# Kernel optimization log

Measured on AMD Instinct MI355X. Metric: run time of the kernel, lower is better.

Reference implementation:

```python
import jax, jax.numpy as jnp
import numpy as np
from jax.scipy.linalg import expm

B_SZ, T, INPUT_D = 32, 1024, 256
MEMORY_D, ORDER, THETA, HIDDEN = 8, 256, 1024.0, 512


def _lmu_matrices(order, theta):
    # Continuous-time Legendre system, then zero-order-hold discretization
    Q = np.arange(order, dtype=np.float64)
    R = (2 * Q + 1)[:, None] / theta
    j, i = np.meshgrid(Q, Q)
    Ac = np.where(i < j, -1.0, (-1.0) ** (i - j + 1)) * R
    Bc = (-1.0) ** Q[:, None] * R
    # ZOH via matrix exponential of the augmented system [[A,B],[0,0]]
    M = np.zeros((order + 1, order + 1))
    M[:order, :order] = Ac
    M[:order, order:] = Bc
    Md = np.asarray(expm(jnp.asarray(M)))
    Ad, Bd = Md[:order, :order], Md[:order, order:]
    # Stored transposed, as in LMUCell.build (used as right-multiplies)
    return Ad.T.astype(np.float32), Bd.T.astype(np.float32)  # (order,order), (1,order)


def setup_inputs() -> dict:
    key = jax.random.key(0)
    k1, k2, k3 = jax.random.split(key, 3)
    A, B = _lmu_matrices(ORDER, THETA)
    hidden_in = MEMORY_D * ORDER
    # glorot-uniform-like scales
    s_k = np.sqrt(6.0 / (INPUT_D + MEMORY_D)).astype(np.float32)
    s_h = np.sqrt(6.0 / (hidden_in + HIDDEN)).astype(np.float32)
    return {
        "x": jax.random.normal(k1, (B_SZ, T, INPUT_D), dtype=jnp.float32),
        "kernel": jax.random.uniform(k2, (INPUT_D, MEMORY_D), jnp.float32, -s_k, s_k),
        "Wh": jax.random.uniform(k3, (hidden_in, HIDDEN), jnp.float32, -s_h, s_h),
        "bh": jnp.zeros((HIDDEN,), jnp.float32),
        "A": jnp.asarray(A),
        "B": jnp.asarray(B),
    }


def reference(x, kernel, Wh, bh, A, B):
    # Encode all timesteps at once: u_t = x_t @ kernel  -> (B, T, memory_d)
    U = jnp.einsum("bti,im->btm", x, kernel)
    m0 = jnp.zeros((x.shape[0], MEMORY_D, ORDER), x.dtype)
    Brow = B[0]  # (order,)

    def step(m, u):
        # m: (B, memory_d, order); per LMUCell: m = m @ A + u[...,None] @ B
        m = jnp.einsum("bdo,op->bdp", m, A) + u[:, :, None] * Brow
        return m, m

    _, ms = jax.lax.scan(step, m0, jnp.swapaxes(U, 0, 1))  # (T, B, md, order)
    ms = jnp.swapaxes(ms, 0, 1).reshape(x.shape[0], x.shape[1], MEMORY_D * ORDER)
    # hidden cell: Dense(tanh) applied to memory at every step (return_sequences)
    return jnp.tanh(ms @ Wh + bh)  # (B, T, HIDDEN)
```

## Files before the change

### kernel.cpp

```cpp
#include <hip/hip_runtime.h>
#include <cstdint>
#include <cstddef>

constexpr int BSZ = 32;
constexpr int T   = 1024;
constexpr int ID  = 256;
constexpr int MD  = 8;
constexpr int ORD = 256;
constexpr int HID = 512;
constexpr int BD  = BSZ * MD;
constexpr int CH  = 64;
constexpr int NQ  = T / CH;
constexpr int DO  = MD * ORD;
constexpr int OO  = ORD * ORD;
constexpr int KTOT24 = CH + ORD;

typedef unsigned short ushort_t;
typedef __attribute__((ext_vector_type(8))) short bf16x8;
typedef __attribute__((ext_vector_type(8))) unsigned short us8;
typedef __attribute__((ext_vector_type(4))) float f32x4;

__device__ inline ushort_t f2bf(float f) {
    union { float f; uint32_t u; } v; v.f = f;
    uint32_t r = v.u + 0x7fffu + ((v.u >> 16) & 1u);
    return (ushort_t)(r >> 16);
}

__device__ inline void gl_lds16(const void* g, void* l) {
    __builtin_amdgcn_global_load_lds(
        (const __attribute__((address_space(1))) void*)g,
        (__attribute__((address_space(3))) void*)l, 16, 0, 0);
}

constexpr size_t AL = 256;
constexpr size_t alup(size_t x) { return (x + AL - 1) & ~(AL - 1); }
constexpr size_t OFF_U2   = 0;
constexpr size_t OFF_P    = alup(OFF_U2   + (size_t)BD * T * 4);
constexpr size_t OFF_APOW = alup(OFF_P    + (size_t)CH * ORD * 4);
constexpr size_t OFF_MQ   = alup(OFF_APOW + (size_t)(CH + 1) * OO * 4);
constexpr size_t OFF_LEND = alup(OFF_MQ   + (size_t)NQ * BD * ORD * 4);
constexpr size_t OFF_U2B  = alup(OFF_LEND + (size_t)NQ * BD * ORD * 4);
constexpr size_t OFF_PTRB = alup(OFF_U2B  + (size_t)BD * T * 2);
constexpr size_t OFF_APB  = alup(OFF_PTRB + (size_t)CH * ORD * CH * 2);
constexpr size_t OFF_WHBT = alup(OFF_APB  + (size_t)CH * ORD * ORD * 2);
constexpr size_t OFF_MQB  = alup(OFF_WHBT + (size_t)HID * DO * 2);
constexpr size_t OFF_MBUF = alup(OFF_MQB  + (size_t)NQ * BD * ORD * 2);

__global__ __launch_bounds__(256) void k_prep0(const float* __restrict__ x,
                                               const float* __restrict__ kern,
                                               float* __restrict__ U2,
                                               ushort_t* __restrict__ U2b,
                                               const float* __restrict__ A,
                                               float* __restrict__ Apow,
                                               ushort_t* __restrict__ Apb,
                                               const float* __restrict__ Wh,
                                               ushort_t* __restrict__ Whbt,
                                               const float* __restrict__ Brow,
                                               float* __restrict__ P) {
    __shared__ __align__(16) char sm[32 * (ID + 1) * 4 + ID * MD * 4];
    const int bid = blockIdx.x;
    const int tid = threadIdx.x;

    if (bid < 1024) {
        float (*xs)[ID + 1] = (float (*)[ID + 1])sm;
        float (*ks)[MD]     = (float (*)[MD])(sm + 32 * (ID + 1) * 4);
        const int b  = bid / (T / 32);
        const int t0 = (bid % (T / 32)) * 32;
        for (int i = tid; i < ID * MD; i += 256) ks[i / MD][i % MD] = kern[i];
        const float* xp = x + ((size_t)b * T + t0) * ID;
        for (int i = tid; i < (32 * ID) / 4; i += 256) {
            float4 v = ((const float4*)xp)[i];
            int r = i >> 6, c = (i & 63) * 4;
            xs[r][c] = v.x; xs[r][c + 1] = v.y; xs[r][c + 2] = v.z; xs[r][c + 3] = v.w;
        }
        __syncthreads();
        const int d  = tid / 32;
        const int tl = tid % 32;
        float acc = 0.f;
        #pragma unroll 8
        for (int i = 0; i < ID; ++i) acc += xs[tl][i] * ks[i][d];
        size_t idx = ((size_t)b * MD + d) * T + t0 + tl;
        U2[idx]  = acc;
        U2b[idx] = f2bf(acc);
    } else if (bid < 1088) {
        float (*t)[33] = (float (*)[33])sm;
        const int i2 = bid - 1024;
        const int o0 = (i2 & 7) * 32, p0 = (i2 >> 3) * 32;
        const int tx = tid & 31, ty = tid >> 5;
        #pragma unroll
        for (int p = 0; p < 4; ++p) {
            int r = ty + p * 8;
            float v = A[(size_t)(p0 + r) * ORD + o0 + tx];
            Apow[OO + (size_t)(p0 + r) * ORD + o0 + tx] = v;
            t[r][tx] = v;
        }
        __syncthreads();
        #pragma unroll
        for (int p = 0; p < 4; ++p) {
            int r = ty + p * 8;
            Apb[(size_t)(o0 + r) * ORD + p0 + tx] = f2bf(t[tx][r]);
        }
    } else if (bid < 2112) {
        float (*t)[33] = (float (*)[33])sm;
        const int i2 = bid - 1088;
        const int k0 = (i2 & 63) * 32, h0 = (i2 >> 6) * 32;
        const int tx = tid & 31, ty = tid >> 5;
        #pragma unroll
        for (int p = 0; p < 4; ++p) {
            int r = ty + p * 8;
            t[r][tx] = Wh[(size_t)(k0 + r) * HID + h0 + tx];
        }
        __syncthreads();
        #pragma unroll
        for (int p = 0; p < 4; ++p) {
            int r = ty + p * 8;
            Whbt[(size_t)(h0 + r) * DO + k0 + tx] = f2bf(t[tx][r]);
        }
    } else {
        P[tid] = Brow[tid];
    }
}


__device__ void pow_body(char* sm, int bid, int tid,
                         float* Apow, ushort_t* Apb, int n) {
    float (*As)[132] = (float (*)[132])sm;
    float (*Bs)[68]  = (float (*)[68])(sm + 33792);
    ushort_t (*tr)[72] = (ushort_t (*)[72])(sm + 68608);
    const int z    = bid >> 4;
    const int row0 = ((bid >> 2) & 3) * 64;
    const int col0 = (bid & 3) * 64;
    const int tx = tid & 15, ty = tid >> 4;
    const float* Ag = Apow + (size_t)(z + 1) * OO;
    const float* Bg = Apow + (size_t)n * OO;
    float*       Cg = Apow + (size_t)(n + z + 1) * OO;

    float acc[4][4] = {};
    for (int k0 = 0; k0 < ORD; k0 += 128) {
        for (int i = tid; i < 64 * 32; i += 256) {
            int m = i >> 5, kv = (i & 31) * 4;
            *(float4*)&As[m][kv] =
                *(const float4*)&Ag[(size_t)(row0 + m) * ORD + k0 + kv];
        }
        for (int i = tid; i < 128 * 16; i += 256) {
            int kk = i >> 4, nv = (i & 15) * 4;
            *(float4*)&Bs[kk][nv] =
                *(const float4*)&Bg[(size_t)(k0 + kk) * ORD + col0 + nv];
        }
        __syncthreads();
        for (int kk = 0; kk < 128; ++kk) {
            float a[4], b[4];
            #pragma unroll
            for (int i = 0; i < 4; ++i) a[i] = As[ty * 4 + i][kk];
            #pragma unroll
            for (int j = 0; j < 4; ++j) b[j] = Bs[kk][tx * 4 + j];
            #pragma unroll
            for (int i = 0; i < 4; ++i)
                #pragma unroll
                for (int j = 0; j < 4; ++j) acc[i][j] += a[i] * b[j];
        }
        __syncthreads();
    }
    ushort_t* ap = Apb + (size_t)(n + z) * OO;
    #pragma unroll
    for (int i = 0; i < 4; ++i) {
        float4 v = make_float4(acc[i][0], acc[i][1], acc[i][2], acc[i][3]);
        *(float4*)&Cg[(size_t)(row0 + ty * 4 + i) * ORD + col0 + tx * 4] = v;
        #pragma unroll
        for (int j = 0; j < 4; ++j)
            tr[tx * 4 + j][ty * 4 + i] = f2bf(acc[i][j]);
    }
    __syncthreads();
    #pragma unroll
    for (int i = 0; i < 2; ++i) {
        int u = tid + i * 256;
        int cc = u >> 3, seg = (u & 7) * 8;
        *(us8*)&ap[(size_t)(col0 + cc) * ORD + row0 + seg] =
            *(const us8*)&tr[cc][seg];
    }
}

__global__ __launch_bounds__(256) void k_pow_w(float* __restrict__ Apow,
                                               ushort_t* __restrict__ Apb,
                                               float* __restrict__ P, int n) {
    __shared__ __align__(16) char sm[77824];
    const int bid = blockIdx.x;
    const int tid = threadIdx.x;
    if (bid < 16 * n) { pow_body(sm, bid, tid, Apow, Apb, n); return; }
    float* br = (float*)sm;
    const int j = bid - 16 * n;
    const int o = tid;
    br[o] = P[(size_t)j * ORD + o];
    __syncthreads();
    const float* M = Apow + (size_t)n * OO;
    float acc = 0.f;
    #pragma unroll 8
    for (int op = 0; op < ORD; ++op) acc += br[op] * M[(size_t)op * ORD + o];
    P[(size_t)(n + j) * ORD + o] = acc;
}

__device__ void prep1_body(char* sm, int bid, int tid,
                           const float* P, ushort_t* Ptrib,
                           const float* U2, float* Lend, float* MqA) {
    if (bid < 256) {
        ushort_t (*tile)[72] = (ushort_t (*)[72])sm;
        const int c  = bid >> 2;
        const int ob = (bid & 3) * 64;
        const int o  = tid & 63;
        const int j4 = tid >> 6;
        for (int jj = j4; jj < CH; jj += 4) {
            float v = (jj <= c) ? P[(size_t)(c - jj) * ORD + ob + o] : 0.f;
            tile[o][jj] = f2bf(v);
        }
        __syncthreads();
        #pragma unroll
        for (int i = 0; i < 2; ++i) {
            int u = tid + i * 256;
            int ol = u >> 3, seg = (u & 7) * 8;
            *(us8*)&Ptrib[((size_t)(c * ORD + ob + ol)) * CH + seg] =
                *(const us8*)&tile[ol][seg];
        }
    } else {
        float (*As)[68] = (float (*)[68])sm;
        float (*Bs)[68] = (float (*)[68])(sm + 17408);
        const int i2   = bid - 256;
        const int col0 = (i2 & 3) * 64;
        const int row0 = ((i2 >> 2) & 3) * 64;
        const int q    = i2 >> 4;
        const int tx = tid & 15, ty = tid >> 4;

        for (int i = tid; i < 64 * 16; i += 256) {
            int m = i >> 4, kv = (i & 15) * 4;
            *(float4*)&As[m][kv] =
                *(const float4*)&U2[(size_t)(row0 + m) * T + q * CH + kv];
        }
        for (int i = tid; i < 64 * 16; i += 256) {
            int kk = i >> 4, nv = (i & 15) * 4;
            *(float4*)&Bs[kk][nv] =
                *(const float4*)&P[(size_t)(CH - 1 - kk) * ORD + col0 + nv];
        }
        __syncthreads();
        float acc[4][4] = {};
        for (int kk = 0; kk < 64; ++kk) {
            float a[4], b[4];
            #pragma unroll
            for (int i = 0; i < 4; ++i) a[i] = As[ty * 4 + i][kk];
            #pragma unroll
            for (int j = 0; j < 4; ++j) b[j] = Bs[kk][tx * 4 + j];
            #pragma unroll
            for (int i = 0; i < 4; ++i)
                #pragma unroll
                for (int j = 0; j < 4; ++j) acc[i][j] += a[i] * b[j];
        }
        __syncthreads();
        #pragma unroll
        for (int i = 0; i < 4; ++i) {
            float4 v = make_float4(acc[i][0], acc[i][1], acc[i][2], acc[i][3]);
            size_t off = (size_t)(row0 + ty * 4 + i) * ORD + col0 + tx * 4;
            *(float4*)&Lend[(size_t)q * (BD * ORD) + off] = v;
            if (q + 1 < NQ) *(float4*)&MqA[(size_t)(q + 1) * (BD * ORD) + off] = v;
            if (q == 0) {
                float4 z = make_float4(0.f, 0.f, 0.f, 0.f);
                *(float4*)&MqA[off] = z;
            }
        }
    }
}

__global__ __launch_bounds__(256) void k_prep1_w(const float* __restrict__ P,
                                                 ushort_t* __restrict__ Ptrib,
                                                 const float* __restrict__ U2,
                                                 float* __restrict__ Lend,
                                                 float* __restrict__ MqA) {
    __shared__ __align__(16) char sm[34816];
    prep1_body(sm, blockIdx.x, threadIdx.x, P, Ptrib, U2, Lend, MqA);
}

__device__ void scan_body(char* sm, int bid, int tid,
                          const float* Min, float* Mout, const float* Pw,
                          int stride, ushort_t* dstb, float* Pnext) {
    float (*As)[132] = (float (*)[132])sm;
    float (*Bs)[68]  = (float (*)[68])(sm + 33792);
    const int tx = tid & 15, ty = tid >> 4;

    if (bid >= 256) {
        if (!Pnext || bid >= 272) return;
        const int i3 = bid - 256;
        const int row0 = (i3 >> 2) * 64;
        const int col0 = (i3 & 3) * 64;
        float acc[4][4] = {};
        for (int k0 = 0; k0 < ORD; k0 += 128) {
            for (int i = tid; i < 64 * 32; i += 256) {
                int m = i >> 5, kv = (i & 31) * 4;
                *(float4*)&As[m][kv] =
                    *(const float4*)&Pw[(size_t)(row0 + m) * ORD + k0 + kv];
            }
            for (int i = tid; i < 128 * 16; i += 256) {
                int kk = i >> 4, nv = (i & 15) * 4;
                *(float4*)&Bs[kk][nv] =
                    *(const float4*)&Pw[(size_t)(k0 + kk) * ORD + col0 + nv];
            }
            __syncthreads();
            for (int kk = 0; kk < 128; ++kk) {
                float a[4], b[4];
                #pragma unroll
                for (int i = 0; i < 4; ++i) a[i] = As[ty * 4 + i][kk];
                #pragma unroll
                for (int j = 0; j < 4; ++j) b[j] = Bs[kk][tx * 4 + j];
                #pragma unroll
                for (int i = 0; i < 4; ++i)
                    #pragma unroll
                    for (int j = 0; j < 4; ++j) acc[i][j] += a[i] * b[j];
            }
            __syncthreads();
        }
        #pragma unroll
        for (int i = 0; i < 4; ++i) {
            float4 v = make_float4(acc[i][0], acc[i][1], acc[i][2], acc[i][3]);
            *(float4*)&Pnext[(size_t)(row0 + ty * 4 + i) * ORD + col0 + tx * 4] = v;
        }
        return;
    }

    const int q    = bid >> 4;
    const int row0 = ((bid >> 2) & 3) * 64;
    const int col0 = (bid & 3) * 64;
    const float* src = Min + (size_t)q * (BD * ORD);
    float*       dst = Mout + (size_t)q * (BD * ORD);
    ushort_t*    db  = dstb ? dstb + (size_t)q * (BD * ORD) : nullptr;

    if (q - stride < 1) {
        for (int i = tid; i < 64 * 64; i += 256) {
            int r = i >> 6, c = i & 63;
            size_t off = (size_t)(row0 + r) * ORD + col0 + c;
            float v = src[off];
            if (db) db[off] = f2bf(v); else dst[off] = v;
        }
        return;
    }

    const float* Ag = Min + (size_t)(q - stride) * (BD * ORD);
    float acc[4][4] = {};
    for (int k0 = 0; k0 < ORD; k0 += 128) {
        for (int i = tid; i < 64 * 32; i += 256) {
            int m = i >> 5, kv = (i & 31) * 4;
            *(float4*)&As[m][kv] =
                *(const float4*)&Ag[(size_t)(row0 + m) * ORD + k0 + kv];
        }
        for (int i = tid; i < 128 * 16; i += 256) {
            int kk = i >> 4, nv = (i & 15) * 4;
            *(float4*)&Bs[kk][nv] =
                *(const float4*)&Pw[(size_t)(k0 + kk) * ORD + col0 + nv];
        }
        __syncthreads();
        for (int kk = 0; kk < 128; ++kk) {
            float a[4], b[4];
            #pragma unroll
            for (int i = 0; i < 4; ++i) a[i] = As[ty * 4 + i][kk];
            #pragma unroll
            for (int j = 0; j < 4; ++j) b[j] = Bs[kk][tx * 4 + j];
            #pragma unroll
            for (int i = 0; i < 4; ++i)
                #pragma unroll
                for (int j = 0; j < 4; ++j) acc[i][j] += a[i] * b[j];
        }
        __syncthreads();
    }
    #pragma unroll
    for (int i = 0; i < 4; ++i) {
        int row = row0 + ty * 4 + i;
        #pragma unroll
        for (int j = 0; j < 4; ++j) {
            int o = col0 + tx * 4 + j;
            size_t off = (size_t)row * ORD + o;
            float val = acc[i][j] + src[off];
            if (db) db[off] = f2bf(val); else dst[off] = val;
        }
    }
}

__global__ __launch_bounds__(256) void k_scan_w(const float* __restrict__ Min,
                                                float* __restrict__ Mout,
                                                const float* __restrict__ Pw,
                                                int stride,
                                                ushort_t* __restrict__ dstb,
                                                float* __restrict__ Pnext) {
    __shared__ __align__(16) char sm[68608];
    scan_body(sm, blockIdx.x, threadIdx.x, Min, Mout, Pw, stride, dstb, Pnext);
}

__global__ __launch_bounds__(256) void k_gemm24(const ushort_t* __restrict__ U2b,
                                                const ushort_t* __restrict__ Mqb,
                                                const ushort_t* __restrict__ Ptrib,
                                                const ushort_t* __restrict__ Apb,
                                                ushort_t* __restrict__ mbuf,
                                                int gbase, int nrows) {
    __shared__ __align__(16) char sm[128 * 136 * 2];
    ushort_t* As = (ushort_t*)sm;
    ushort_t* Bs = As + 128 * 64;
    ushort_t (*st)[136] = (ushort_t (*)[136])sm;
    const int q       = blockIdx.z;
    const int rowbase = blockIdx.y * 128;
    const int colbase = blockIdx.x * 128;
    const int tid  = threadIdx.x;
    const int lane = tid & 63;
    const int wid  = tid >> 6;
    const int wr = wid >> 1, wc = wid & 1;
    const int lr = lane & 15, hi = lane >> 4;

    f32x4 acc[4][4];
    #pragma unroll
    for (int m = 0; m < 4; ++m)
        #pragma unroll
        for (int n = 0; n < 4; ++n) acc[m][n] = 0.f;

    for (int s = 0; s < KTOT24 / 64; ++s) {
        const int k0 = s * 64;
        #pragma unroll
        for (int i = 0; i < 4; ++i) {
            const int ub = (wid * 4 + i) * 64;
            const int u  = ub + lane;
            const int row = u >> 3;
            const int sw  = (((u & 7) ^ (row & 7))) * 8;
            int gr = rowbase + row;
            if (gr >= nrows) gr = nrows - 1;
            const ushort_t *ga, *gb;
            if (s == 0) {
                ga = &U2b[(size_t)(gbase + gr) * T + q * CH + sw];
                gb = &Ptrib[(size_t)(colbase + row) * CH + sw];
            } else {
                ga = &Mqb[((size_t)q * BD + gbase + gr) * ORD + (k0 - CH) + sw];
                gb = &Apb[(size_t)(colbase + row) * ORD + (k0 - CH) + sw];
            }
            gl_lds16(ga, &As[ub * 8]);
            gl_lds16(gb, &Bs[ub * 8]);
        }
        __syncthreads();
        #pragma unroll
        for (int t = 0; t < 2; ++t) {
            bf16x8 af[4], bfv[4];
            #pragma unroll
            for (int m = 0; m < 4; ++m) {
                int r = wr * 64 + m * 16 + lr;
                int un = (t * 4 + hi) ^ (r & 7);
                af[m] = *(const bf16x8*)&As[r * 64 + un * 8];
            }
            #pragma unroll
            for (int n = 0; n < 4; ++n) {
                int r = wc * 64 + n * 16 + lr;
                int un = (t * 4 + hi) ^ (r & 7);
                bfv[n] = *(const bf16x8*)&Bs[r * 64 + un * 8];
            }
            #pragma unroll
            for (int m = 0; m < 4; ++m)
                #pragma unroll
                for (int n = 0; n < 4; ++n)
                    acc[m][n] = __builtin_amdgcn_mfma_f32_16x16x32_bf16(af[m], bfv[n], acc[m][n], 0, 0, 0);
        }
        __syncthreads();
    }

    #pragma unroll
    for (int m = 0; m < 4; ++m)
        #pragma unroll
        for (int n = 0; n < 4; ++n)
            #pragma unroll
            for (int r = 0; r < 4; ++r)
                st[wr * 64 + m * 16 + hi * 4 + r]
                  [wc * 64 + n * 16 + lr] = f2bf(acc[m][n][r]);
    __syncthreads();

    const int c     = colbase >> 8;
    const int obase = colbase & 255;
    #pragma unroll
    for (int i = 0; i < 8; ++i) {
        int u  = tid + i * 256;
        int rl = u >> 4, cb = (u & 15) * 8;
        int grow = rowbase + rl;
        if (grow < nrows) {
            int bl = grow >> 3, d = grow & 7;
            size_t addr = ((size_t)(bl * T + q * CH + c)) * DO + (d << 8) + obase + cb;
            *(us8*)&mbuf[addr] = *(const us8*)&st[rl][cb];
        }
    }
}

__global__ __launch_bounds__(512) void k_gemm5(const ushort_t* __restrict__ mbuf,
                                               const ushort_t* __restrict__ Whbt,
                                               const float* __restrict__ bh,
                                               float* __restrict__ out, int np) {
    __shared__ ushort_t A4[4][256 * 32];
    __shared__ ushort_t B4[4][256 * 32];
    const int nwg = np * 2;
    int wg = blockIdx.x;
    int bx, by;
    if ((nwg & 7) == 0 && (np & 3) == 0) {
        int xcd = wg & 7, j = wg >> 3;
        bx = j & 1;
        by = xcd * (np >> 3) + (j >> 1);
    } else { bx = wg & 1; by = wg >> 1; }
    const int rowbase = by * 256;
    const int colbase = bx * 256;
    const int tid  = threadIdx.x;
    const int lane = tid & 63;
    const int wid  = tid >> 6;
    const int wr = wid >> 2, wcw = wid & 3;
    const int lr = lane & 15, hi = lane >> 4;

    f32x4 acc[8][4];
    #pragma unroll
    for (int m = 0; m < 8; ++m)
        #pragma unroll
        for (int n = 0; n < 4; ++n) acc[m][n] = 0.f;

    const int NT = DO / 32;

    auto STAGE_A = [&](int s) {
        const int k0 = s * 32;
        ushort_t* slot = A4[s & 3];
        #pragma unroll
        for (int i = 0; i < 2; ++i) {
            const int ug = i * 512 + wid * 64;
            const int u  = ug + lane;
            const int row = u >> 2, uu = u & 3;
            const int col = k0 + ((uu ^ ((row >> 1) & 3)) * 8);
            gl_lds16(&mbuf[(size_t)(rowbase + row) * DO + col], &slot[ug * 8]);
        }
    };
    auto STAGE_B = [&](int s) {
        const int k0 = s * 32;
        ushort_t* slot = B4[s & 3];
        #pragma unroll
        for (int i = 0; i < 2; ++i) {
            const int ug = i * 512 + wid * 64;
            const int u  = ug + lane;
            const int row = u >> 2, uu = u & 3;
            const int col = k0 + ((uu ^ ((row >> 1) & 3)) * 8);
            gl_lds16(&Whbt[(size_t)(colbase + row) * DO + col], &slot[ug * 8]);
        }
    };

    STAGE_A(0); STAGE_B(0);
    STAGE_A(1); STAGE_B(1);
    STAGE_A(2); STAGE_B(2);
    asm volatile("s_waitcnt vmcnt(8)" ::: "memory");
    __builtin_amdgcn_s_barrier();

    for (int k = 0; k < NT; ++k) {
        const int sl = k & 3;
        ushort_t* As_ = A4[sl];
        ushort_t* Bs_ = B4[sl];
        bf16x8 bv[4], av[4];

        #pragma unroll
        for (int n = 0; n < 4; ++n) {
            int r = wcw * 64 + n * 16 + lr;
            bv[n] = *(const bf16x8*)&Bs_[r * 32 + ((hi ^ ((r >> 1) & 3)) * 8)];
        }
        #pragma unroll
        for (int m = 0; m < 4; ++m) {
            int r = wr * 128 + m * 16 + lr;
            av[m] = *(const bf16x8*)&As_[r * 32 + ((hi ^ ((r >> 1) & 3)) * 8)];
        }
        if (k + 3 < NT) STAGE_A(k + 3);
        __builtin_amdgcn_s_barrier();
        __builtin_amdgcn_s_setprio(1);
        #pragma unroll
        for (int m = 0; m < 4; ++m)
            #pragma unroll
            for (int n = 0; n < 4; ++n)
                acc[m][n] = __builtin_amdgcn_mfma_f32_16x16x32_bf16(av[m], bv[n], acc[m][n], 0, 0, 0);
        __builtin_amdgcn_s_setprio(0);

        #pragma unroll
        for (int m = 0; m < 4; ++m) {
            int r = wr * 128 + 64 + m * 16 + lr;
            av[m] = *(const bf16x8*)&As_[r * 32 + ((hi ^ ((r >> 1) & 3)) * 8)];
        }
        if (k + 3 < NT) STAGE_B(k + 3);
        __builtin_amdgcn_s_setprio(1);
        #pragma unroll
        for (int m = 0; m < 4; ++m)
            #pragma unroll
            for (int n = 0; n < 4; ++n)
                acc[4 + m][n] = __builtin_amdgcn_mfma_f32_16x16x32_bf16(av[m], bv[n], acc[4 + m][n], 0, 0, 0);
        __builtin_amdgcn_s_setprio(0);

        if (k < NT - 1) {
            if (k < NT - 3)       asm volatile("s_waitcnt vmcnt(8)" ::: "memory");
            else if (k == NT - 3) asm volatile("s_waitcnt vmcnt(4)" ::: "memory");
            else                  asm volatile("s_waitcnt vmcnt(0)" ::: "memory");
            __builtin_amdgcn_s_barrier();
        }
    }

    #pragma unroll
    for (int m = 0; m < 8; ++m) {
        #pragma unroll
        for (int n = 0; n < 4; ++n) {
            int col = colbase + wcw * 64 + n * 16 + lr;
            float bias = bh[col];
            #pragma unroll
            for (int r = 0; r < 4; ++r) {
                int grow = rowbase + wr * 128 + m * 16 + hi * 4 + r;
                out[(size_t)grow * HID + col] = tanhf(acc[m][n][r] + bias);
            }
        }
    }
}

extern "C" void kernel_launch(void* const* d_in, const int* in_sizes, int n_in,
                              void* d_out, int out_size, void* d_ws, size_t ws_size,
                              hipStream_t stream) {
    const float* x    = (const float*)d_in[0];
    const float* kern = (const float*)d_in[1];
    const float* Wh   = (const float*)d_in[2];
    const float* bh   = (const float*)d_in[3];
    const float* A    = (const float*)d_in[4];
    const float* Brow = (const float*)d_in[5];
    float* out = (float*)d_out;

    char* base = (char*)d_ws;
    float*    U2    = (float*)(base + OFF_U2);
    float*    P     = (float*)(base + OFF_P);
    float*    Apow  = (float*)(base + OFF_APOW);
    float*    MqA   = (float*)(base + OFF_MQ);
    float*    Lend  = (float*)(base + OFF_LEND);
    ushort_t* U2b   = (ushort_t*)(base + OFF_U2B);
    ushort_t* Ptrib = (ushort_t*)(base + OFF_PTRB);
    ushort_t* Apb   = (ushort_t*)(base + OFF_APB);
    ushort_t* Whbt  = (ushort_t*)(base + OFF_WHBT);
    ushort_t* Mqb   = (ushort_t*)(base + OFF_MQB);
    ushort_t* mbuf  = (ushort_t*)(base + OFF_MBUF);

    float* A64  = Apow + (size_t)CH * OO;
    float* A128 = Apow;
    float* A256 = U2;
    float* A512 = U2 + OO;

    int G = 1;
    for (int g = 32; g >= 1; g >>= 1) {
        if (OFF_MBUF + (size_t)g * T * DO * 2 <= ws_size) { G = g; break; }
    }
    const int ngroups = BSZ / G;

    k_prep0<<<dim3(2113), 256, 0, stream>>>(
        x, kern, U2, U2b, A, Apow, Apb, Wh, Whbt, Brow, P);

    for (int n = 1; n < CH; n <<= 1)
        k_pow_w<<<dim3(17 * n), 256, 0, stream>>>(Apow, Apb, P, n);

    k_prep1_w<<<dim3(512), 256, 0, stream>>>(P, Ptrib, U2, Lend, MqA);

    k_scan_w<<<dim3(272), 256, 0, stream>>>(MqA, Lend, A64, 1, nullptr, A128);
    k_scan_w<<<dim3(272), 256, 0, stream>>>(Lend, MqA, A128, 2, nullptr, A256);
    k_scan_w<<<dim3(272), 256, 0, stream>>>(MqA, Lend, A256, 4, nullptr, A512);
    k_scan_w<<<dim3(256), 256, 0, stream>>>(Lend, MqA, A512, 8, Mqb, nullptr);

    for (int g = 0; g < ngroups; ++g) {
        const int gbase = g * G * MD;
        const int nrows = G * MD;
        const int gy24  = (nrows + 127) / 128;
        k_gemm24<<<dim3((CH * ORD) / 128, gy24, NQ), 256, 0, stream>>>(
            U2b, Mqb, Ptrib, Apb, mbuf, gbase, nrows);
        const int np = (G * T) / 256;
        k_gemm5<<<dim3(np * 2), 512, 0, stream>>>(
            mbuf, Whbt, bh, out + (size_t)g * G * T * HID, np);
    }
}
```

Baseline: 343.1 us.

## Fuse power, prep and scan stages into one persistent kernel with flag dataflow

Replaces the sequence of k_pow_w launches, k_prep1_w and four k_scan_w launches with a single persistent 256-block kernel. Work units are sequenced by uid and synchronized with global atomic counters (acquire/release spin-waits), so dependent tiles can start as soon as their inputs are ready instead of waiting for full kernel boundaries. This removes about ten launch gaps and tail idleness. In exchange it adds spin-wait overhead and relies on the in-order uid assignment to avoid deadlock. The Lend/MqA write pattern is also restructured.

```diff
diff --git a/kernel.cpp b/kernel.cpp
--- a/kernel.cpp
+++ b/kernel.cpp
@@ -44,7 +44,23 @@
 constexpr size_t OFF_APB  = alup(OFF_PTRB + (size_t)CH * ORD * CH * 2);
 constexpr size_t OFF_WHBT = alup(OFF_APB  + (size_t)CH * ORD * ORD * 2);
 constexpr size_t OFF_MQB  = alup(OFF_WHBT + (size_t)HID * DO * 2);
-constexpr size_t OFF_MBUF = alup(OFF_MQB  + (size_t)NQ * BD * ORD * 2);
+constexpr size_t OFF_FLG  = alup(OFF_MQB  + (size_t)NQ * BD * ORD * 2);
+constexpr size_t OFF_MBUF = alup(OFF_FLG  + 1024);
+
+__device__ inline void gwait(uint32_t* f, uint32_t want) {
+    if (threadIdx.x == 0) {
+        while (__hip_atomic_load(f, __ATOMIC_ACQUIRE,
+                                 __HIP_MEMORY_SCOPE_AGENT) < want)
+            __builtin_amdgcn_s_sleep(4);
+    }
+    __syncthreads();
+}
+__device__ inline void gpost(uint32_t* f, uint32_t v) {
+    __syncthreads();
+    if (threadIdx.x == 0)
+        __hip_atomic_fetch_add(f, v, __ATOMIC_RELEASE,
+                               __HIP_MEMORY_SCOPE_AGENT);
+}
 
 __global__ __launch_bounds__(256) void k_prep0(const float* __restrict__ x,
                                                const float* __restrict__ kern,
@@ -56,7 +72,8 @@
                                                const float* __restrict__ Wh,
                                                ushort_t* __restrict__ Whbt,
                                                const float* __restrict__ Brow,
-                                               float* __restrict__ P) {
+                                               float* __restrict__ P,
+                                               uint32_t* __restrict__ F) {
     __shared__ __align__(16) char sm[32 * (ID + 1) * 4 + ID * MD * 4];
     const int bid = blockIdx.x;
     const int tid = threadIdx.x;
@@ -117,19 +134,20 @@
             Whbt[(size_t)(h0 + r) * DO + k0 + tx] = f2bf(t[tx][r]);
         }
     } else {
+        F[tid] = 0u;
+        __syncthreads();
+        if (tid == 0) { F[1] = 16u; F[65] = 1u; }
         P[tid] = Brow[tid];
     }
 }
 
 
-__device__ void pow_body(char* sm, int bid, int tid,
+__device__ void pow_unit(char* sm, int z, int ry, int cx, int tid,
                          float* Apow, ushort_t* Apb, int n) {
     float (*As)[132] = (float (*)[132])sm;
     float (*Bs)[68]  = (float (*)[68])(sm + 33792);
     ushort_t (*tr)[72] = (ushort_t (*)[72])(sm + 68608);
-    const int z    = bid >> 4;
-    const int row0 = ((bid >> 2) & 3) * 64;
-    const int col0 = (bid & 3) * 64;
+    const int row0 = ry * 64, col0 = cx * 64;
     const int tx = tid & 15, ty = tid >> 4;
     const float* Ag = Apow + (size_t)(z + 1) * OO;
     const float* Bg = Apow + (size_t)n * OO;
@@ -180,15 +198,9 @@
     }
 }
 
-__global__ __launch_bounds__(256) void k_pow_w(float* __restrict__ Apow,
-                                               ushort_t* __restrict__ Apb,
-                                               float* __restrict__ P, int n) {
-    __shared__ __align__(16) char sm[77824];
-    const int bid = blockIdx.x;
-    const int tid = threadIdx.x;
-    if (bid < 16 * n) { pow_body(sm, bid, tid, Apow, Apb, n); return; }
+__device__ void p_double(char* sm, int j, int n, int tid,
+                         const float* Apow, float* P) {
     float* br = (float*)sm;
-    const int j = bid - 16 * n;
     const int o = tid;
     br[o] = P[(size_t)j * ORD + o];
     __syncthreads();
@@ -197,51 +209,97 @@
     #pragma unroll 8
     for (int op = 0; op < ORD; ++op) acc += br[op] * M[(size_t)op * ORD + o];
     P[(size_t)(n + j) * ORD + o] = acc;
-}
-
-__device__ void prep1_body(char* sm, int bid, int tid,
-                           const float* P, ushort_t* Ptrib,
-                           const float* U2, float* Lend, float* MqA) {
-    if (bid < 256) {
-        ushort_t (*tile)[72] = (ushort_t (*)[72])sm;
-        const int c  = bid >> 2;
-        const int ob = (bid & 3) * 64;
-        const int o  = tid & 63;
-        const int j4 = tid >> 6;
-        for (int jj = j4; jj < CH; jj += 4) {
-            float v = (jj <= c) ? P[(size_t)(c - jj) * ORD + ob + o] : 0.f;
-            tile[o][jj] = f2bf(v);
-        }
-        __syncthreads();
-        #pragma unroll
-        for (int i = 0; i < 2; ++i) {
-            int u = tid + i * 256;
-            int ol = u >> 3, seg = (u & 7) * 8;
-            *(us8*)&Ptrib[((size_t)(c * ORD + ob + ol)) * CH + seg] =
-                *(const us8*)&tile[ol][seg];
-        }
-    } else {
-        float (*As)[68] = (float (*)[68])sm;
-        float (*Bs)[68] = (float (*)[68])(sm + 17408);
-        const int i2   = bid - 256;
-        const int col0 = (i2 & 3) * 64;
-        const int row0 = ((i2 >> 2) & 3) * 64;
-        const int q    = i2 >> 4;
-        const int tx = tid & 15, ty = tid >> 4;
-
-        for (int i = tid; i < 64 * 16; i += 256) {
-            int m = i >> 4, kv = (i & 15) * 4;
+    __syncthreads();
+}
+
+__device__ void ptrib_unit(char* sm, int L, int tid,
+                           const float* P, ushort_t* Ptrib) {
+    ushort_t (*tile)[72] = (ushort_t (*)[72])sm;
+    const int c  = L >> 2;
+    const int ob = (L & 3) * 64;
+    const int o  = tid & 63;
+    const int j4 = tid >> 6;
+    for (int jj = j4; jj < CH; jj += 4) {
+        float v = (jj <= c) ? P[(size_t)(c - jj) * ORD + ob + o] : 0.f;
+        tile[o][jj] = f2bf(v);
+    }
+    __syncthreads();
+    #pragma unroll
+    for (int i = 0; i < 2; ++i) {
+        int u = tid + i * 256;
+        int ol = u >> 3, seg = (u & 7) * 8;
+        *(us8*)&Ptrib[((size_t)(c * ORD + ob + ol)) * CH + seg] =
+            *(const us8*)&tile[ol][seg];
+    }
+    __syncthreads();
+}
+
+__device__ void lend_unit(char* sm, int i2, int tid,
+                          const float* U2, const float* P, float* MqA) {
+    float (*As)[68] = (float (*)[68])sm;
+    float (*Bs)[68] = (float (*)[68])(sm + 17408);
+    const int col0 = (i2 & 3) * 64;
+    const int row0 = ((i2 >> 2) & 3) * 64;
+    const int q    = i2 >> 4;
+    const int tx = tid & 15, ty = tid >> 4;
+
+    for (int i = tid; i < 64 * 16; i += 256) {
+        int m = i >> 4, kv = (i & 15) * 4;
+        *(float4*)&As[m][kv] =
+            *(const float4*)&U2[(size_t)(row0 + m) * T + q * CH + kv];
+    }
+    for (int i = tid; i < 64 * 16; i += 256) {
+        int kk = i >> 4, nv = (i & 15) * 4;
+        *(float4*)&Bs[kk][nv] =
+            *(const float4*)&P[(size_t)(CH - 1 - kk) * ORD + col0 + nv];
+    }
+    __syncthreads();
+    float acc[4][4] = {};
+    for (int kk = 0; kk < 64; ++kk) {
+        float a[4], b[4];
+        #pragma unroll
+        for (int i = 0; i < 4; ++i) a[i] = As[ty * 4 + i][kk];
+        #pragma unroll
+        for (int j = 0; j < 4; ++j) b[j] = Bs[kk][tx * 4 + j];
+        #pragma unroll
+        for (int i = 0; i < 4; ++i)
+            #pragma unroll
+            for (int j = 0; j < 4; ++j) acc[i][j] += a[i] * b[j];
+    }
+    __syncthreads();
+    #pragma unroll
+    for (int i = 0; i < 4; ++i) {
+        float4 v = make_float4(acc[i][0], acc[i][1], acc[i][2], acc[i][3]);
+        size_t off = (size_t)(row0 + ty * 4 + i) * ORD + col0 + tx * 4;
+        *(float4*)&MqA[(size_t)(q + 1) * (BD * ORD) + off] = v;
+        if (q == 0) {
+            float4 z = make_float4(0.f, 0.f, 0.f, 0.f);
+            *(float4*)&MqA[off] = z;
+        }
+    }
+}
+
+__device__ void sq_unit(char* sm, int t, int tid,
+                        const float* X, float* Cdst) {
+    float (*As)[132] = (float (*)[132])sm;
+    float (*Bs)[68]  = (float (*)[68])(sm + 33792);
+    const int row0 = (t >> 2) * 64;
+    const int col0 = (t & 3) * 64;
+    const int tx = tid & 15, ty = tid >> 4;
+    float acc[4][4] = {};
+    for (int k0 = 0; k0 < ORD; k0 += 128) {
+        for (int i = tid; i < 64 * 32; i += 256) {
+            int m = i >> 5, kv = (i & 31) * 4;
             *(float4*)&As[m][kv] =
-                *(const float4*)&U2[(size_t)(row0 + m) * T + q * CH + kv];
-        }
-        for (int i = tid; i < 64 * 16; i += 256) {
+                *(const float4*)&X[(size_t)(row0 + m) * ORD + k0 + kv];
+        }
+        for (int i = tid; i < 128 * 16; i += 256) {
             int kk = i >> 4, nv = (i & 15) * 4;
             *(float4*)&Bs[kk][nv] =
-                *(const float4*)&P[(size_t)(CH - 1 - kk) * ORD + col0 + nv];
-        }
-        __syncthreads();
-        float acc[4][4] = {};
-        for (int kk = 0; kk < 64; ++kk) {
+                *(const float4*)&X[(size_t)(k0 + kk) * ORD + col0 + nv];
+        }
+        __syncthreads();
+        for (int kk = 0; kk < 128; ++kk) {
             float a[4], b[4];
             #pragma unroll
             for (int i = 0; i < 4; ++i) a[i] = As[ty * 4 + i][kk];
@@ -253,80 +311,24 @@
                 for (int j = 0; j < 4; ++j) acc[i][j] += a[i] * b[j];
         }
         __syncthreads();
-        #pragma unroll
-        for (int i = 0; i < 4; ++i) {
-            float4 v = make_float4(acc[i][0], acc[i][1], acc[i][2], acc[i][3]);
-            size_t off = (size_t)(row0 + ty * 4 + i) * ORD + col0 + tx * 4;
-            *(float4*)&Lend[(size_t)q * (BD * ORD) + off] = v;
-            if (q + 1 < NQ) *(float4*)&MqA[(size_t)(q + 1) * (BD * ORD) + off] = v;
-            if (q == 0) {
-                float4 z = make_float4(0.f, 0.f, 0.f, 0.f);
-                *(float4*)&MqA[off] = z;
-            }
-        }
-    }
-}
-
-__global__ __launch_bounds__(256) void k_prep1_w(const float* __restrict__ P,
-                                                 ushort_t* __restrict__ Ptrib,
-                                                 const float* __restrict__ U2,
-                                                 float* __restrict__ Lend,
-                                                 float* __restrict__ MqA) {
-    __shared__ __align__(16) char sm[34816];
-    prep1_body(sm, blockIdx.x, threadIdx.x, P, Ptrib, U2, Lend, MqA);
-}
-
-__device__ void scan_body(char* sm, int bid, int tid,
+    }
+    #pragma unroll
+    for (int i = 0; i < 4; ++i) {
+        float4 v = make_float4(acc[i][0], acc[i][1], acc[i][2], acc[i][3]);
+        *(float4*)&Cdst[(size_t)(row0 + ty * 4 + i) * ORD + col0 + tx * 4] = v;
+    }
+}
+
+__device__ void scan_unit(char* sm, int q, int t, int tid,
                           const float* Min, float* Mout, const float* Pw,
-                          int stride, ushort_t* dstb, float* Pnext) {
+                          int stride, ushort_t* dstb) {
     float (*As)[132] = (float (*)[132])sm;
     float (*Bs)[68]  = (float (*)[68])(sm + 33792);
+    const int row0 = ((t >> 2) & 3) * 64;
+    const int col0 = (t & 3) * 64;
     const int tx = tid & 15, ty = tid >> 4;
-
-    if (bid >= 256) {
-        if (!Pnext || bid >= 272) return;
-        const int i3 = bid - 256;
-        const int row0 = (i3 >> 2) * 64;
-        const int col0 = (i3 & 3) * 64;
-        float acc[4][4] = {};
-        for (int k0 = 0; k0 < ORD; k0 += 128) {
-            for (int i = tid; i < 64 * 32; i += 256) {
-                int m = i >> 5, kv = (i & 31) * 4;
-                *(float4*)&As[m][kv] =
-                    *(const float4*)&Pw[(size_t)(row0 + m) * ORD + k0 + kv];
-            }
-            for (int i = tid; i < 128 * 16; i += 256) {
-                int kk = i >> 4, nv = (i & 15) * 4;
-                *(float4*)&Bs[kk][nv] =
-                    *(const float4*)&Pw[(size_t)(k0 + kk) * ORD + col0 + nv];
-            }
-            __syncthreads();
-            for (int kk = 0; kk < 128; ++kk) {
-                float a[4], b[4];
-                #pragma unroll
-                for (int i = 0; i < 4; ++i) a[i] = As[ty * 4 + i][kk];
-                #pragma unroll
-                for (int j = 0; j < 4; ++j) b[j] = Bs[kk][tx * 4 + j];
-                #pragma unroll
-                for (int i = 0; i < 4; ++i)
-                    #pragma unroll
-                    for (int j = 0; j < 4; ++j) acc[i][j] += a[i] * b[j];
-            }
-            __syncthreads();
-        }
-        #pragma unroll
-        for (int i = 0; i < 4; ++i) {
-            float4 v = make_float4(acc[i][0], acc[i][1], acc[i][2], acc[i][3]);
-            *(float4*)&Pnext[(size_t)(row0 + ty * 4 + i) * ORD + col0 + tx * 4] = v;
-        }
-        return;
-    }
-
-    const int q    = bid >> 4;
-    const int row0 = ((bid >> 2) & 3) * 64;
-    const int col0 = (bid & 3) * 64;
     const float* src = Min + (size_t)q * (BD * ORD);
-    float*       dst = Mout + (size_t)q * (BD * ORD);
+    float*       dst = Mout ? Mout + (size_t)q * (BD * ORD) : nullptr;
     ushort_t*    db  = dstb ? dstb + (size_t)q * (BD * ORD) : nullptr;
 
     if (q - stride < 1) {
@@ -336,6 +338,7 @@
             float v = src[off];
             if (db) db[off] = f2bf(v); else dst[off] = v;
         }
+        __syncthreads();
         return;
     }
 
@@ -377,16 +380,104 @@
             if (db) db[off] = f2bf(val); else dst[off] = val;
         }
     }
-}
-
-__global__ __launch_bounds__(256) void k_scan_w(const float* __restrict__ Min,
-                                                float* __restrict__ Mout,
-                                                const float* __restrict__ Pw,
-                                                int stride,
-                                                ushort_t* __restrict__ dstb,
-                                                float* __restrict__ Pnext) {
-    __shared__ __align__(16) char sm[68608];
-    scan_body(sm, blockIdx.x, threadIdx.x, Min, Mout, Pw, stride, dstb, Pnext);
+    __syncthreads();
+}
+
+__global__ __launch_bounds__(256) void k_midp(float* __restrict__ Apow,
+                                              ushort_t* __restrict__ Apb,
+                                              float* __restrict__ P,
+                                              ushort_t* __restrict__ Ptrib,
+                                              const float* __restrict__ U2,
+                                              float* __restrict__ MqA,
+                                              float* __restrict__ Lend,
+                                              ushort_t* __restrict__ Mqb,
+                                              float* __restrict__ A128,
+                                              float* __restrict__ A256,
+                                              float* __restrict__ A512,
+                                              uint32_t* __restrict__ F) {
+    __shared__ __align__(16) char sm[77824];
+    const int tid = threadIdx.x;
+    float* A64 = Apow + (size_t)CH * OO;
+
+    for (int uid = blockIdx.x; uid < 2655; uid += 256) {
+        if (uid < 1071) {
+            int n, base;
+            if      (uid < 17)  { n = 1;  base = 0;   }
+            else if (uid < 51)  { n = 2;  base = 17;  }
+            else if (uid < 119) { n = 4;  base = 51;  }
+            else if (uid < 255) { n = 8;  base = 119; }
+            else if (uid < 527) { n = 16; base = 255; }
+            else                { n = 32; base = 527; }
+            int L = uid - base;
+            if (L < 16 * n) {
+                int z = L >> 4, t = L & 15;
+                gwait(F + (z + 1), 16);
+                gwait(F + n, 16);
+                pow_unit(sm, z, (t >> 2) & 3, t & 3, tid, Apow, Apb, n);
+                gpost(F + (n + z + 1), 1);
+            } else {
+                int j = L - 16 * n;
+                gwait(F + 65, (uint32_t)n);
+                gwait(F + n, 16);
+                p_double(sm, j, n, tid, Apow, P);
+                gpost(F + 65, 1);
+            }
+        } else if (uid < 1583) {
+            int L = uid - 1071;
+            gwait(F + 65, 64);
+            if (L < 256) {
+                ptrib_unit(sm, L, tid, P, Ptrib);
+            } else {
+                int i2 = L - 256;
+                int q = i2 >> 4;
+                if (q < 15) {
+                    lend_unit(sm, i2, tid, U2, P, MqA);
+                    gpost(F + 70 + (q + 1), 1);
+                    if (q == 0) gpost(F + 70 + 0, 1);
+                    gpost(F + 66, 1);
+                }
+            }
+        } else if (uid < 1599) {
+            gwait(F + 64, 16);
+            sq_unit(sm, uid - 1583, tid, A64, A128);
+            gpost(F + 67, 1);
+        } else if (uid < 1855) {
+            int L = uid - 1599; int q = L >> 4; int t = L & 15;
+            gwait(F + 70 + q, 16);
+            if (q - 1 >= 1) { gwait(F + 70 + (q - 1), 16); gwait(F + 64, 16); }
+            scan_unit(sm, q, t, tid, MqA, Lend, A64, 1, nullptr);
+            gpost(F + 86 + q, 1);
+        } else if (uid < 1871) {
+            gwait(F + 67, 16);
+            gwait(F + 66, 240);
+            sq_unit(sm, uid - 1855, tid, A128, A256);
+            gpost(F + 68, 1);
+        } else if (uid < 2127) {
+            int L = uid - 1871; int q = L >> 4; int t = L & 15;
+            gwait(F + 86 + q, 16);
+            if (q + 1 <= 15) gwait(F + 86 + (q + 1), 16);
+            if (q - 2 >= 1) { gwait(F + 86 + (q - 2), 16); gwait(F + 67, 16); }
+            scan_unit(sm, q, t, tid, Lend, MqA, A128, 2, nullptr);
+            gpost(F + 102 + q, 1);
+        } else if (uid < 2143) {
+            gwait(F + 68, 16);
+            gwait(F + 66, 240);
+            sq_unit(sm, uid - 2127, tid, A256, A512);
+            gpost(F + 69, 1);
+        } else if (uid < 2399) {
+            int L = uid - 2143; int q = L >> 4; int t = L & 15;
+            gwait(F + 102 + q, 16);
+            if (q + 2 <= 15) gwait(F + 102 + (q + 2), 16);
+            if (q - 4 >= 1) { gwait(F + 102 + (q - 4), 16); gwait(F + 68, 16); }
+            scan_unit(sm, q, t, tid, MqA, Lend, A256, 4, nullptr);
+            gpost(F + 118 + q, 1);
+        } else {
+            int L = uid - 2399; int q = L >> 4; int t = L & 15;
+            gwait(F + 118 + q, 16);
+            if (q - 8 >= 1) { gwait(F + 118 + (q - 8), 16); gwait(F + 69, 16); }
+            scan_unit(sm, q, t, tid, Lend, nullptr, A512, 8, Mqb);
+        }
+    }
 }
 
 __global__ __launch_bounds__(256) void k_gemm24(const ushort_t* __restrict__ U2b,
@@ -631,9 +722,9 @@
     ushort_t* Apb   = (ushort_t*)(base + OFF_APB);
     ushort_t* Whbt  = (ushort_t*)(base + OFF_WHBT);
     ushort_t* Mqb   = (ushort_t*)(base + OFF_MQB);
+    uint32_t* F     = (uint32_t*)(base + OFF_FLG);
     ushort_t* mbuf  = (ushort_t*)(base + OFF_MBUF);
 
-    float* A64  = Apow + (size_t)CH * OO;
     float* A128 = Apow;
     float* A256 = U2;
     float* A512 = U2 + OO;
@@ -645,17 +736,10 @@
     const int ngroups = BSZ / G;
 
     k_prep0<<<dim3(2113), 256, 0, stream>>>(
-        x, kern, U2, U2b, A, Apow, Apb, Wh, Whbt, Brow, P);
-
-    for (int n = 1; n < CH; n <<= 1)
-        k_pow_w<<<dim3(17 * n), 256, 0, stream>>>(Apow, Apb, P, n);
-
-    k_prep1_w<<<dim3(512), 256, 0, stream>>>(P, Ptrib, U2, Lend, MqA);
-
-    k_scan_w<<<dim3(272), 256, 0, stream>>>(MqA, Lend, A64, 1, nullptr, A128);
-    k_scan_w<<<dim3(272), 256, 0, stream>>>(Lend, MqA, A128, 2, nullptr, A256);
-    k_scan_w<<<dim3(272), 256, 0, stream>>>(MqA, Lend, A256, 4, nullptr, A512);
-    k_scan_w<<<dim3(256), 256, 0, stream>>>(Lend, MqA, A512, 8, Mqb, nullptr);
+        x, kern, U2, U2b, A, Apow, Apb, Wh, Whbt, Brow, P, F);
+
+    k_midp<<<dim3(256), 256, 0, stream>>>(
+        Apow, Apb, P, Ptrib, U2, MqA, Lend, Mqb, A128, A256, A512, F);
 
     for (int g = 0; g < ngroups; ++g) {
         const int gbase = g * G * MD;
```

Result: slower. 790.5 us (+130.4%).
